# Kernel tuning notes

Hardware: AMD Instinct MI355X
Metric: run time of the kernel (lower is better)

The kernel has to match this reference:

```python
import jax, jax.numpy as jnp
import numpy as np

B, S, N, F, H, E, L = 16, 64, 128, 16, 64, 1024, 2
NEG_SLOPE = 0.2


def _gat_layer(h, src, tgt, Wl, bl, Wr, br, att, bo):
    # h: [B,S,N,H]; src/tgt: [Et] (edges incl. self-loops)
    xl = jnp.einsum('bsnf,hf->bsnh', h, Wl) + bl
    xr = jnp.einsum('bsnf,hf->bsnh', h, Wr) + br
    e = xl[:, :, src] + xr[:, :, tgt]                       # [B,S,Et,H]
    e = jnp.where(e > 0, e, NEG_SLOPE * e)                  # leaky_relu(0.2)
    a = jnp.einsum('bseh,h->bse', e, att)                   # [B,S,Et]
    # segment softmax over target node (stable)
    m = jnp.full(a.shape[:2] + (N,), -jnp.inf, a.dtype).at[:, :, tgt].max(a)
    p = jnp.exp(a - m[:, :, tgt])
    z = jnp.zeros(a.shape[:2] + (N,), a.dtype).at[:, :, tgt].add(p)
    alpha = p / z[:, :, tgt]
    out = jnp.zeros_like(xl).at[:, :, tgt].add(alpha[..., None] * xl[:, :, src])
    return out + bo


def _forward(x, edge_index, in_W, in_b, gat_Wl, gat_bl, gat_Wr, gat_br,
             gat_att, gat_bias, gru_Wih, gru_Whh, gru_bih, gru_bhh,
             oh_W1, oh_b1, oh_W2, oh_b2, dh_W1, dh_b1, dh_W2, dh_b2):
    ar = jnp.arange(N, dtype=edge_index.dtype)
    ei = jnp.concatenate([edge_index, jnp.stack([ar, ar])], axis=1)  # add self-loops
    src, tgt = ei[0], ei[1]
    h = jnp.einsum('bsnf,hf->bsnh', x, in_W) + in_b          # input_proj
    for l in range(L):
        h = jax.nn.relu(_gat_layer(h, src, tgt, gat_Wl[l], gat_bl[l],
                                   gat_Wr[l], gat_br[l], gat_att[l], gat_bias[l]))
    # [B,S,N,H] -> sequences [B*N, S, H]; GRU, keep last state
    seqs = h.transpose(0, 2, 1, 3).reshape(B * N, S, H)

    def step(hprev, xt):
        gi = xt @ gru_Wih.T + gru_bih
        gh = hprev @ gru_Whh.T + gru_bhh
        ir, iz, inn = jnp.split(gi, 3, axis=-1)
        hr, hz, hn = jnp.split(gh, 3, axis=-1)
        r = jax.nn.sigmoid(ir + hr)
        zz = jax.nn.sigmoid(iz + hz)
        n = jnp.tanh(inn + r * hn)
        hnew = (1 - zz) * n + zz * hprev
        return hnew, None

    h0 = jnp.zeros((B * N, H), h.dtype)
    h_last, _ = jax.lax.scan(step, h0, seqs.transpose(1, 0, 2))
    h_last = h_last.reshape(B, N, H)

    def head(hh, W1, b1, W2, b2):
        return jax.nn.relu(hh @ W1.T + b1) @ W2.T + b2

    order = head(h_last, oh_W1, oh_b1, oh_W2, oh_b2)        # [B,N,1]
    demand = head(h_last, dh_W1, dh_b1, dh_W2, dh_b2)       # [B,N,1]
    return order, demand


def setup_inputs() -> dict:
    key = jax.random.key(0)
    ks = jax.random.split(key, 16)
    def g(i, shp, s=0.05):
        return (jax.random.normal(ks[i], shp) * s).astype(jnp.float32)
    x = jax.random.normal(ks[0], (B, S, N, F), dtype=jnp.float32)
    src = jax.random.randint(ks[1], (E,), 0, N)
    off = jax.random.randint(ks[2], (E,), 1, N)
    edge_index = jnp.stack([src, (src + off) % N]).astype(jnp.int32)  # no self-loops
    zf = lambda shp: jnp.zeros(shp, jnp.float32)
    return dict(
        x=x, edge_index=edge_index,
        in_W=g(3, (H, F)), in_b=zf((H,)),
        gat_Wl=g(4, (L, H, H)), gat_bl=zf((L, H)),
        gat_Wr=g(5, (L, H, H)), gat_br=zf((L, H)),
        gat_att=g(6, (L, H), 0.1), gat_bias=zf((L, H)),
        gru_Wih=g(7, (3 * H, H)), gru_Whh=g(8, (3 * H, H)),
        gru_bih=zf((3 * H,)), gru_bhh=zf((3 * H,)),
        oh_W1=g(9, (H // 2, H)), oh_b1=zf((H // 2,)),
        oh_W2=g(10, (1, H // 2)), oh_b2=zf((1,)),
        dh_W1=g(11, (H // 2, H)), dh_b1=zf((H // 2,)),
        dh_W2=g(12, (1, H // 2)), dh_b2=zf((1,)),
    )


def reference(x, edge_index, in_W, in_b, gat_Wl, gat_bl, gat_Wr, gat_br,
              gat_att, gat_bias, gru_Wih, gru_Whh, gru_bih, gru_bhh,
              oh_W1, oh_b1, oh_W2, oh_b2, dh_W1, dh_b1, dh_W2, dh_b2):
    return _forward(x, edge_index, in_W, in_b, gat_Wl, gat_bl, gat_Wr, gat_br,
                    gat_att, gat_bias, gru_Wih, gru_Whh, gru_bih, gru_bhh,
                    oh_W1, oh_b1, oh_W2, oh_b2, dh_W1, dh_b1, dh_W2, dh_b2)
```

## Files before the change

kernel.cpp:

```cpp
#include <hip/hip_runtime.h>
#include <math.h>

#define BB 16
#define SS 64
#define NN 128
#define FF 16
#define HH 64
#define EE 1024
#define ET 1152
#define LLAYERS 2
#define XPAD 65
#define RT (BB * SS * NN)

__device__ __forceinline__ float readlane_f(float v, int k) {
  return __int_as_float(__builtin_amdgcn_readlane(__float_as_int(v), k));
}
__device__ __forceinline__ unsigned flipf(float f) {
  unsigned u = __float_as_uint(f);
  unsigned mask = (u & 0x80000000u) ? 0xFFFFFFFFu : 0x80000000u;
  return u ^ mask;
}
__device__ __forceinline__ float unflipf(unsigned u) {
  unsigned b = (u & 0x80000000u) ? (u ^ 0x80000000u) : ~u;
  return __uint_as_float(b);
}
__device__ __forceinline__ float sigmoidf_(float x) { return 1.f / (1.f + expf(-x)); }

__global__ void setup_csr_kernel(const int* __restrict__ ei,
                                 int* __restrict__ off,
                                 int* __restrict__ csrc,
                                 int* __restrict__ ctgt) {
  __shared__ int deg[NN], cur[NN], offs[NN + 1];
  int tid = threadIdx.x;
  if (tid < NN) deg[tid] = 0;
  __syncthreads();
  for (int e = tid; e < ET; e += 256) {
    int tg = (e < EE) ? ei[EE + e] : (e - EE);
    atomicAdd(&deg[tg], 1);
  }
  __syncthreads();
  if (tid == 0) {
    int s = 0;
    for (int i = 0; i < NN; ++i) { offs[i] = s; s += deg[i]; }
    offs[NN] = s;
  }
  __syncthreads();
  if (tid < NN) cur[tid] = offs[tid];
  if (tid <= NN) off[tid] = offs[tid];
  __syncthreads();
  for (int e = tid; e < ET; e += 256) {
    int sv, tg;
    if (e < EE) { sv = ei[e]; tg = ei[EE + e]; }
    else        { sv = e - EE; tg = e - EE; }
    int pos = atomicAdd(&cur[tg], 1);
    csrc[pos] = sv;
    ctgt[pos] = tg;
  }
}

__global__ __launch_bounds__(256) void input_proj_kernel(
    const float* __restrict__ x, const float* __restrict__ W,
    const float* __restrict__ bvec, float* __restrict__ h) {
  int lane = threadIdx.x & 63;
  int wid = threadIdx.x >> 6;
  float wreg[FF];
#pragma unroll
  for (int i = 0; i < FF / 4; ++i)
    *(float4*)&wreg[4 * i] = ((const float4*)(W + lane * FF))[i];
  float bias = bvec[lane];
  int row0 = __builtin_amdgcn_readfirstlane((blockIdx.x * 4 + wid) * 32);
#pragma unroll 2
  for (int r = 0; r < 32; ++r) {
    int row = row0 + r;
    const float* xr = x + row * FF;
    float acc = bias;
#pragma unroll
    for (int f = 0; f < FF; ++f) acc += xr[f] * wreg[f];
    h[row * HH + lane] = acc;
  }
}

__global__ __launch_bounds__(256) void xlxr_kernel(
    const float* __restrict__ hin,
    const float* __restrict__ Wl, const float* __restrict__ bl,
    const float* __restrict__ Wr, const float* __restrict__ br,
    float* __restrict__ xl, float* __restrict__ xr) {
  int lane = threadIdx.x & 63;
  int wid = (int)threadIdx.x >> 6;
  const float* W  = (wid & 1) ? Wr : Wl;
  const float* bv = (wid & 1) ? br : bl;
  float* outp     = (wid & 1) ? xr : xl;
  float w[HH];
#pragma unroll
  for (int i = 0; i < HH / 4; ++i)
    *(float4*)&w[4 * i] = ((const float4*)(W + lane * HH))[i];
  float bias = bv[lane];
  int row0 = __builtin_amdgcn_readfirstlane(blockIdx.x * 64 + (wid >> 1) * 32);
#pragma unroll 2
  for (int r = 0; r < 32; ++r) {
    const float* hrow = hin + (size_t)(row0 + r) * HH;
    float a0 = bias, a1 = 0.f, a2 = 0.f, a3 = 0.f;
#pragma unroll
    for (int f = 0; f < HH; f += 4) {
      a0 += hrow[f + 0] * w[f + 0];
      a1 += hrow[f + 1] * w[f + 1];
      a2 += hrow[f + 2] * w[f + 2];
      a3 += hrow[f + 3] * w[f + 3];
    }
    outp[(size_t)(row0 + r) * HH + lane] = (a0 + a1) + (a2 + a3);
  }
}

__global__ __launch_bounds__(256) void gat_edge_kernel(
    const float* __restrict__ xl_g, const float* __restrict__ xr_g,
    float* __restrict__ hout,
    const int* __restrict__ csr_off, const int* __restrict__ csr_src,
    const int* __restrict__ csr_tgt,
    const float* __restrict__ att, const float* __restrict__ bo) {
  __shared__ float xl_sh[NN * XPAD];
  __shared__ float xr_sh[NN * XPAD];
  __shared__ float p_sh[ET];
  __shared__ int st_sh[ET];
  __shared__ unsigned m_sh[NN];
  int tid = threadIdx.x, lane = tid & 63, wid = tid >> 6;
  int base = blockIdx.x * (NN * HH);

#pragma unroll 1
  for (int i = tid * 4; i < NN * HH; i += 256 * 4) {
    int row = i >> 6, h = i & 63;
    float4 vl = *(const float4*)(xl_g + base + i);
    float4 vr = *(const float4*)(xr_g + base + i);
    float* dl = xl_sh + row * XPAD + h;
    float* dr = xr_sh + row * XPAD + h;
    dl[0] = vl.x; dl[1] = vl.y; dl[2] = vl.z; dl[3] = vl.w;
    dr[0] = vr.x; dr[1] = vr.y; dr[2] = vr.z; dr[3] = vr.w;
  }
  for (int i = tid; i < ET; i += 256)
    st_sh[i] = csr_src[i] | (csr_tgt[i] << 16);
  if (tid < NN) m_sh[tid] = 0u;
  __syncthreads();

#pragma unroll 1
  for (int e = tid; e < ET; e += 256) {
    int st = st_sh[e];
    int s = st & 0xffff, tg = st >> 16;
    const float* xlr = xl_sh + s * XPAD;
    const float* xrr = xr_sh + tg * XPAD;
    float a0 = 0.f, a1 = 0.f, a2 = 0.f, a3 = 0.f;
#pragma unroll
    for (int h = 0; h < HH; h += 4) {
      float v0 = xlr[h + 0] + xrr[h + 0]; v0 = (v0 > 0.f) ? v0 : 0.2f * v0;
      float v1 = xlr[h + 1] + xrr[h + 1]; v1 = (v1 > 0.f) ? v1 : 0.2f * v1;
      float v2 = xlr[h + 2] + xrr[h + 2]; v2 = (v2 > 0.f) ? v2 : 0.2f * v2;
      float v3 = xlr[h + 3] + xrr[h + 3]; v3 = (v3 > 0.f) ? v3 : 0.2f * v3;
      a0 += v0 * att[h + 0];
      a1 += v1 * att[h + 1];
      a2 += v2 * att[h + 2];
      a3 += v3 * att[h + 3];
    }
    float a = (a0 + a1) + (a2 + a3);
    p_sh[e] = a;
    atomicMax(&m_sh[tg], flipf(a));
  }
  __syncthreads();

  for (int e = tid; e < ET; e += 256) {
    int tg = st_sh[e] >> 16;
    p_sh[e] = expf(p_sh[e] - unflipf(m_sh[tg]));
  }
  __syncthreads();

  float bo_l = bo[lane];
#pragma unroll 1
  for (int n = wid; n < NN; n += 4) {
    int o0 = __builtin_amdgcn_readfirstlane(csr_off[n]);
    int o1 = __builtin_amdgcn_readfirstlane(csr_off[n + 1]);
    float acc = 0.f, z = 0.f;
    for (int i = o0; i < o1; ++i) {
      float p = p_sh[i];
      int s = st_sh[i] & 0xffff;
      acc += p * xl_sh[s * XPAD + lane];
      z += p;
    }
    float o = acc / z + bo_l;
    hout[base + n * HH + lane] = fmaxf(o, 0.f);
  }
}

__device__ __forceinline__ void gemm_half(
    const float* __restrict__ hin, int base,
    const float* __restrict__ W, const float* __restrict__ bvec,
    float* __restrict__ out_sh, int half, int lane) {
  float wreg[HH];
#pragma unroll
  for (int i = 0; i < HH / 4; ++i)
    *(float4*)&wreg[4 * i] = ((const float4*)(W + lane * HH))[i];
  float bias = bvec[lane];
  int n0 = __builtin_amdgcn_readfirstlane(half * 64);
#pragma unroll 1
  for (int nd = 0; nd < 64; ++nd) {
    int node = n0 + nd;
    const float* hrow = hin + base + node * HH;
    float a0 = bias, a1 = 0.f, a2 = 0.f, a3 = 0.f;
#pragma unroll
    for (int f = 0; f < HH; f += 4) {
      a0 += hrow[f + 0] * wreg[f + 0];
      a1 += hrow[f + 1] * wreg[f + 1];
      a2 += hrow[f + 2] * wreg[f + 2];
      a3 += hrow[f + 3] * wreg[f + 3];
    }
    out_sh[node * HH + lane] = (a0 + a1) + (a2 + a3);
  }
}

__global__ __launch_bounds__(256) void gat_fused_kernel(
    const float* __restrict__ hin, float* __restrict__ hout,
    const int* __restrict__ csr_off, const int* __restrict__ csr_src,
    const int* __restrict__ csr_tgt,
    const float* __restrict__ Wl, const float* __restrict__ bl,
    const float* __restrict__ Wr, const float* __restrict__ br,
    const float* __restrict__ att, const float* __restrict__ bo) {
  __shared__ float xl_sh[NN * HH];
  __shared__ float xr_sh[NN * HH];
  __shared__ float p_sh[ET];
  __shared__ int st_sh[ET];
  __shared__ unsigned m_sh[NN];
  int tid = threadIdx.x, lane = tid & 63, wid = tid >> 6;
  int base = blockIdx.x * (NN * HH);

  for (int i = tid; i < ET; i += 256)
    st_sh[i] = csr_src[i] | (csr_tgt[i] << 16);
  if (tid < NN) m_sh[tid] = 0u;

  if (wid < 2) gemm_half(hin, base, Wl, bl, xl_sh, wid & 1, lane);
  else         gemm_half(hin, base, Wr, br, xr_sh, wid & 1, lane);

  float att_l = att[lane];
  float bo_l = bo[lane];
  __syncthreads();

#pragma unroll 1
  for (int e = wid; e < ET; e += 4) {
    int st = st_sh[e];
    int s = st & 0xffff, tg = st >> 16;
    float v = xl_sh[s * HH + lane] + xr_sh[tg * HH + lane];
    v = (v > 0.f) ? v : 0.2f * v;
    float prod = v * att_l;
#pragma unroll
    for (int mm = 32; mm; mm >>= 1) prod += __shfl_xor(prod, mm);
    if (lane == 0) {
      p_sh[e] = prod;
      atomicMax(&m_sh[tg], flipf(prod));
    }
  }
  __syncthreads();

  for (int e = tid; e < ET; e += 256) {
    int tg = st_sh[e] >> 16;
    p_sh[e] = expf(p_sh[e] - unflipf(m_sh[tg]));
  }
  __syncthreads();

#pragma unroll 1
  for (int n = wid; n < NN; n += 4) {
    int o0 = csr_off[n], o1 = csr_off[n + 1];
    float acc = 0.f, z = 0.f;
    for (int i = o0; i < o1; ++i) {
      float p = p_sh[i];
      int s = st_sh[i] & 0xffff;
      acc += p * xl_sh[s * HH + lane];
      z += p;
    }
    float o = acc / z + bo_l;
    hout[base + n * HH + lane] = fmaxf(o, 0.f);
  }
}

__global__ __launch_bounds__(192) void gi_proj_kernel(
    const float* __restrict__ hin, const float* __restrict__ Wih,
    const float* __restrict__ bih, float* __restrict__ gi) {
  int lane = threadIdx.x & 63;
  int w = (int)threadIdx.x >> 6;
  float wreg[HH];
  const float4* wsrc = (const float4*)(Wih + (size_t)(w * 64 + lane) * HH);
#pragma unroll
  for (int i = 0; i < HH / 4; ++i) *(float4*)&wreg[4 * i] = wsrc[i];
  float bias = bih[w * 64 + lane];
  int row0 = __builtin_amdgcn_readfirstlane(blockIdx.x * 64);
#pragma unroll 2
  for (int r = 0; r < 64; ++r) {
    int row = row0 + r;
    const float* hrow = hin + (size_t)row * HH;
    float a0 = bias, a1 = 0.f, a2 = 0.f, a3 = 0.f;
#pragma unroll
    for (int f = 0; f < HH; f += 4) {
      a0 += hrow[f + 0] * wreg[f + 0];
      a1 += hrow[f + 1] * wreg[f + 1];
      a2 += hrow[f + 2] * wreg[f + 2];
      a3 += hrow[f + 3] * wreg[f + 3];
    }
    gi[(size_t)row * 192 + w * 64 + lane] = (a0 + a1) + (a2 + a3);
  }
}

__global__ __launch_bounds__(64, 2) void gru_rec_kernel(
    const float* __restrict__ gi,
    const float* __restrict__ Whh, const float* __restrict__ bhh,
    const float* __restrict__ oW1, const float* __restrict__ ob1,
    const float* __restrict__ oW2, const float* __restrict__ ob2,
    const float* __restrict__ dW1, const float* __restrict__ db1,
    const float* __restrict__ dW2, const float* __restrict__ db2,
    float* __restrict__ out) {
  int lane = threadIdx.x;
  int seq = blockIdx.x;
  int b = seq >> 7, n = seq & (NN - 1);

  float wr[HH], wz[HH], wn[HH];
  {
    const float4* s0 = (const float4*)(Whh + (size_t)(0 * 64 + lane) * HH);
    const float4* s1 = (const float4*)(Whh + (size_t)(1 * 64 + lane) * HH);
    const float4* s2 = (const float4*)(Whh + (size_t)(2 * 64 + lane) * HH);
#pragma unroll
    for (int i = 0; i < HH / 4; ++i) {
      *(float4*)&wr[4 * i] = s0[i];
      *(float4*)&wz[4 * i] = s1[i];
      *(float4*)&wn[4 * i] = s2[i];
    }
  }
  float br_ = bhh[lane], bz_ = bhh[64 + lane], bn_ = bhh[128 + lane];

  const float* gbase = gi + ((size_t)b * SS * NN + (size_t)n) * 192;
  float gir = gbase[lane], giz = gbase[64 + lane], gin = gbase[128 + lane];
  const float* g1 = gbase + (size_t)NN * 192;
  float pir = g1[lane], piz = g1[64 + lane], pin = g1[128 + lane];
  float hj = 0.f;

#pragma unroll 1
  for (int t = 0; t < SS; ++t) {
    float qir = 0.f, qiz = 0.f, qin = 0.f;
    if (t + 2 < SS) {
      const float* g2 = gbase + (size_t)(t + 2) * NN * 192;
      qir = g2[lane]; qiz = g2[64 + lane]; qin = g2[128 + lane];
    }
    float ar0 = br_, ar1 = 0.f, az0 = bz_, az1 = 0.f, an0 = bn_, an1 = 0.f;
#pragma unroll
    for (int k = 0; k < HH; k += 2) {
      float h0 = readlane_f(hj, k), h1 = readlane_f(hj, k + 1);
      ar0 += h0 * wr[k];     az0 += h0 * wz[k];     an0 += h0 * wn[k];
      ar1 += h1 * wr[k + 1]; az1 += h1 * wz[k + 1]; an1 += h1 * wn[k + 1];
    }
    float r  = sigmoidf_(gir + ar0 + ar1);
    float z  = sigmoidf_(giz + az0 + az1);
    float nn_ = tanhf(gin + r * (an0 + an1));
    hj = (1.f - z) * nn_ + z * hj;
    gir = pir; giz = piz; gin = pin;
    pir = qir; piz = qiz; pin = qin;
  }

  int half = lane >> 5, jp = lane & 31;
  const float* W1 = half ? dW1 : oW1;
  const float* b1 = half ? db1 : ob1;
  const float* W2 = half ? dW2 : oW2;
  const float* b2 = half ? db2 : ob2;
  float wv[HH];
#pragma unroll
  for (int i = 0; i < HH / 4; ++i)
    *(float4*)&wv[4 * i] = ((const float4*)(W1 + jp * HH))[i];
  float acc = b1[jp];
#pragma unroll
  for (int k = 0; k < HH; ++k)
    acc += readlane_f(hj, k) * wv[k];
  float val = fmaxf(acc, 0.f) * W2[jp];
  val += __shfl_down(val, 16, 32);
  val += __shfl_down(val, 8, 32);
  val += __shfl_down(val, 4, 32);
  val += __shfl_down(val, 2, 32);
  val += __shfl_down(val, 1, 32);
  if (jp == 0) out[half * (BB * NN) + seq] = val + b2[0];
}

__global__ __launch_bounds__(192, 3) void gru_fused_kernel(
    const float* __restrict__ hbuf,
    const float* __restrict__ Wih, const float* __restrict__ Whh,
    const float* __restrict__ bih, const float* __restrict__ bhh,
    const float* __restrict__ oW1, const float* __restrict__ ob1,
    const float* __restrict__ oW2, const float* __restrict__ ob2,
    const float* __restrict__ dW1, const float* __restrict__ db1,
    const float* __restrict__ dW2, const float* __restrict__ db2,
    float* __restrict__ out) {
  __shared__ float gi_sh[SS * 3 * HH];
  __shared__ float exch[2][3][HH];

  int lane = threadIdx.x & 63;
  int g = (int)threadIdx.x >> 6;
  int seq = blockIdx.x;
  int b = seq >> 7, n = seq & (NN - 1);
  const float* xbase = hbuf + ((size_t)b * SS * NN + (size_t)n) * HH;

  {
    float w[HH];
    const float4* wsrc = (const float4*)(Wih + (size_t)(g * 64 + lane) * HH);
#pragma unroll
    for (int i = 0; i < HH / 4; ++i) *(float4*)&w[4 * i] = wsrc[i];
    float bias = bih[g * 64 + lane];
#pragma unroll 2
    for (int t = 0; t < SS; ++t) {
      const float* xr = xbase + (size_t)t * NN * HH;
      float a0 = bias, a1 = 0.f, a2 = 0.f, a3 = 0.f;
#pragma unroll
      for (int k = 0; k < HH; k += 4) {
        float4 xb = *(const float4*)(xr + k);
        a0 += xb.x * w[k + 0];
        a1 += xb.y * w[k + 1];
        a2 += xb.z * w[k + 2];
        a3 += xb.w * w[k + 3];
      }
      gi_sh[(t * 3 + g) * HH + lane] = (a0 + a1) + (a2 + a3);
    }
  }

  float whh[HH];
  {
    const float4* wsrc = (const float4*)(Whh + (size_t)(g * 64 + lane) * HH);
#pragma unroll
    for (int i = 0; i < HH / 4; ++i) *(float4*)&whh[4 * i] = wsrc[i];
  }
  float bhg = bhh[g * 64 + lane];
  float hj = 0.f;
  __syncthreads();

#pragma unroll 1
  for (int t = 0; t < SS; ++t) {
    float a0 = bhg, a1 = 0.f, a2 = 0.f, a3 = 0.f;
#pragma unroll
    for (int k = 0; k < HH; k += 4) {
      a0 += readlane_f(hj, k + 0) * whh[k + 0];
      a1 += readlane_f(hj, k + 1) * whh[k + 1];
      a2 += readlane_f(hj, k + 2) * whh[k + 2];
      a3 += readlane_f(hj, k + 3) * whh[k + 3];
    }
    float gh = (a0 + a1) + (a2 + a3);
    int slot = t & 1;
    exch[slot][g][lane] = gh;
    __syncthreads();
    float ghr = exch[slot][0][lane];
    float ghz = exch[slot][1][lane];
    float ghn = exch[slot][2][lane];
    float gir = gi_sh[(t * 3 + 0) * HH + lane];
    float giz = gi_sh[(t * 3 + 1) * HH + lane];
    float gin = gi_sh[(t * 3 + 2) * HH + lane];
    float r  = sigmoidf_(gir + ghr);
    float z  = sigmoidf_(giz + ghz);
    float nn_ = tanhf(gin + r * ghn);
    hj = (1.f - z) * nn_ + z * hj;
  }

  if (g == 0) {
    int half = lane >> 5, jp = lane & 31;
    const float* W1 = half ? dW1 : oW1;
    const float* b1 = half ? db1 : ob1;
    const float* W2 = half ? dW2 : oW2;
    const float* b2 = half ? db2 : ob2;
    float wv[HH];
#pragma unroll
    for (int i = 0; i < HH / 4; ++i)
      *(float4*)&wv[4 * i] = ((const float4*)(W1 + jp * HH))[i];
    float acc = b1[jp];
#pragma unroll
    for (int k = 0; k < HH; ++k)
      acc += readlane_f(hj, k) * wv[k];
    float val = fmaxf(acc, 0.f) * W2[jp];
    val += __shfl_down(val, 16, 32);
    val += __shfl_down(val, 8, 32);
    val += __shfl_down(val, 4, 32);
    val += __shfl_down(val, 2, 32);
    val += __shfl_down(val, 1, 32);
    if (jp == 0) out[half * (BB * NN) + seq] = val + b2[0];
  }
}

extern "C" void kernel_launch(void* const* d_in, const int* in_sizes, int n_in,
                              void* d_out, int out_size, void* d_ws, size_t ws_size,
                              hipStream_t stream) {
  const float* x       = (const float*)d_in[0];
  const int*   ei      = (const int*)d_in[1];
  const float* in_W    = (const float*)d_in[2];
  const float* in_b    = (const float*)d_in[3];
  const float* gat_Wl  = (const float*)d_in[4];
  const float* gat_bl  = (const float*)d_in[5];
  const float* gat_Wr  = (const float*)d_in[6];
  const float* gat_br  = (const float*)d_in[7];
  const float* gat_att = (const float*)d_in[8];
  const float* gat_bias= (const float*)d_in[9];
  const float* gru_Wih = (const float*)d_in[10];
  const float* gru_Whh = (const float*)d_in[11];
  const float* gru_bih = (const float*)d_in[12];
  const float* gru_bhh = (const float*)d_in[13];
  const float* oh_W1   = (const float*)d_in[14];
  const float* oh_b1   = (const float*)d_in[15];
  const float* oh_W2   = (const float*)d_in[16];
  const float* oh_b2   = (const float*)d_in[17];
  const float* dh_W1   = (const float*)d_in[18];
  const float* dh_b1   = (const float*)d_in[19];
  const float* dh_W2   = (const float*)d_in[20];
  const float* dh_b2   = (const float*)d_in[21];
  float* out = (float*)d_out;

  char* ws = (char*)d_ws;
  size_t hfloats = (size_t)BB * SS * NN * HH;
  float* hbuf = (float*)ws;
  size_t off_csr = hfloats * sizeof(float);
  size_t off_buf = off_csr + (160 + 2 * ET) * sizeof(int);
  off_buf = (off_buf + 255) & ~(size_t)255;
  int* csr_off = (int*)(ws + off_csr);
  int* csr_src = csr_off + 160;
  int* csr_tgt = csr_src + ET;
  float* xlbuf = (float*)(ws + off_buf);
  float* xrbuf = xlbuf + hfloats;
  size_t need_gat = off_buf + 2 * hfloats * sizeof(float);
  bool big_gat = (ws_size >= need_gat);
  float* gibuf = (float*)(ws + off_buf);
  size_t need_gru = off_buf + (size_t)RT * 192 * sizeof(float);
  bool big_gru = (ws_size >= need_gru);

  setup_csr_kernel<<<1, 256, 0, stream>>>(ei, csr_off, csr_src, csr_tgt);
  input_proj_kernel<<<(BB * SS * NN) / (4 * 32), 256, 0, stream>>>(x, in_W, in_b, hbuf);
  for (int l = 0; l < LLAYERS; ++l) {
    if (big_gat) {
      xlxr_kernel<<<(BB * SS * NN) / 64, 256, 0, stream>>>(
          hbuf, gat_Wl + l * HH * HH, gat_bl + l * HH,
          gat_Wr + l * HH * HH, gat_br + l * HH, xlbuf, xrbuf);
      gat_edge_kernel<<<BB * SS, 256, 0, stream>>>(
          xlbuf, xrbuf, hbuf, csr_off, csr_src, csr_tgt,
          gat_att + l * HH, gat_bias + l * HH);
    } else {
      gat_fused_kernel<<<BB * SS, 256, 0, stream>>>(
          hbuf, hbuf, csr_off, csr_src, csr_tgt,
          gat_Wl + l * HH * HH, gat_bl + l * HH,
          gat_Wr + l * HH * HH, gat_br + l * HH,
          gat_att + l * HH, gat_bias + l * HH);
    }
  }
  if (big_gru) {
    gi_proj_kernel<<<RT / 64, 192, 0, stream>>>(hbuf, gru_Wih, gru_bih, gibuf);
    gru_rec_kernel<<<BB * NN, 64, 0, stream>>>(
        gibuf, gru_Whh, gru_bhh,
        oh_W1, oh_b1, oh_W2, oh_b2, dh_W1, dh_b1, dh_W2, dh_b2, out);
  } else {
    gru_fused_kernel<<<BB * NN, 192, 0, stream>>>(
        hbuf, gru_Wih, gru_Whh, gru_bih, gru_bhh,
        oh_W1, oh_b1, oh_W2, oh_b2, dh_W1, dh_b1, dh_W2, dh_b2, out);
  }
}
```

Before: 750.3 us.

## Stage hidden rows in LDS and compute multiple projections per thread

xlxr and gi_proj kernels now use single-wavefront blocks. Each block stages a 64-row tile of h into shared memory, and each thread holds all weight rows for its output column (both Wl/Wr, or all three GRU gates), so each h element read is reused across several outputs with float4 LDS loads. The GRU recurrence replaces 64 readlane broadcasts per step with a shared-memory h vector plus a barrier per step. The change raises register pressure (up to 192 weight floats per thread) and lowers threads per block, which risks occupancy and spilling.

```diff
diff --git a/kernel.cpp b/kernel.cpp
--- a/kernel.cpp
+++ b/kernel.cpp
@@ -80,34 +80,47 @@
   }
 }
 
-__global__ __launch_bounds__(256) void xlxr_kernel(
+__global__ __launch_bounds__(64, 2) void xlxr_kernel(
     const float* __restrict__ hin,
     const float* __restrict__ Wl, const float* __restrict__ bl,
     const float* __restrict__ Wr, const float* __restrict__ br,
     float* __restrict__ xl, float* __restrict__ xr) {
-  int lane = threadIdx.x & 63;
-  int wid = (int)threadIdx.x >> 6;
-  const float* W  = (wid & 1) ? Wr : Wl;
-  const float* bv = (wid & 1) ? br : bl;
-  float* outp     = (wid & 1) ? xr : xl;
-  float w[HH];
-#pragma unroll
-  for (int i = 0; i < HH / 4; ++i)
-    *(float4*)&w[4 * i] = ((const float4*)(W + lane * HH))[i];
-  float bias = bv[lane];
-  int row0 = __builtin_amdgcn_readfirstlane(blockIdx.x * 64 + (wid >> 1) * 32);
+  __shared__ float hsh[64][HH];
+  int j = threadIdx.x;
+  float wl_[HH], wr_[HH];
+  {
+    const float4* sl = (const float4*)(Wl + (size_t)j * HH);
+    const float4* sr = (const float4*)(Wr + (size_t)j * HH);
+#pragma unroll
+    for (int i = 0; i < HH / 4; ++i) {
+      *(float4*)&wl_[4 * i] = sl[i];
+      *(float4*)&wr_[4 * i] = sr[i];
+    }
+  }
+  float blj = bl[j], brj = br[j];
+  int row0 = blockIdx.x * 64;
+  {
+    const float4* src = (const float4*)(hin + (size_t)row0 * HH);
+    float4* dst = (float4*)hsh;
+#pragma unroll
+    for (int i = 0; i < 16; ++i)
+      dst[i * 64 + j] = src[i * 64 + j];
+  }
+  __syncthreads();
 #pragma unroll 2
-  for (int r = 0; r < 32; ++r) {
-    const float* hrow = hin + (size_t)(row0 + r) * HH;
-    float a0 = bias, a1 = 0.f, a2 = 0.f, a3 = 0.f;
-#pragma unroll
-    for (int f = 0; f < HH; f += 4) {
-      a0 += hrow[f + 0] * w[f + 0];
-      a1 += hrow[f + 1] * w[f + 1];
-      a2 += hrow[f + 2] * w[f + 2];
-      a3 += hrow[f + 3] * w[f + 3];
-    }
-    outp[(size_t)(row0 + r) * HH + lane] = (a0 + a1) + (a2 + a3);
+  for (int r = 0; r < 64; ++r) {
+    float al0 = blj, al1 = 0.f, ar0 = brj, ar1 = 0.f;
+#pragma unroll
+    for (int k = 0; k < HH; k += 4) {
+      float4 hb = *(const float4*)&hsh[r][k];
+      al0 += hb.x * wl_[k + 0]; ar0 += hb.x * wr_[k + 0];
+      al1 += hb.y * wl_[k + 1]; ar1 += hb.y * wr_[k + 1];
+      al0 += hb.z * wl_[k + 2]; ar0 += hb.z * wr_[k + 2];
+      al1 += hb.w * wl_[k + 3]; ar1 += hb.w * wr_[k + 3];
+    }
+    size_t o = (size_t)(row0 + r) * HH + j;
+    xl[o] = al0 + al1;
+    xr[o] = ar0 + ar1;
   }
 }
 
@@ -276,30 +289,48 @@
   }
 }
 
-__global__ __launch_bounds__(192) void gi_proj_kernel(
+__global__ __launch_bounds__(64, 2) void gi_proj_kernel(
     const float* __restrict__ hin, const float* __restrict__ Wih,
     const float* __restrict__ bih, float* __restrict__ gi) {
-  int lane = threadIdx.x & 63;
-  int w = (int)threadIdx.x >> 6;
-  float wreg[HH];
-  const float4* wsrc = (const float4*)(Wih + (size_t)(w * 64 + lane) * HH);
-#pragma unroll
-  for (int i = 0; i < HH / 4; ++i) *(float4*)&wreg[4 * i] = wsrc[i];
-  float bias = bih[w * 64 + lane];
-  int row0 = __builtin_amdgcn_readfirstlane(blockIdx.x * 64);
+  __shared__ float hsh[64][HH];
+  int j = threadIdx.x;
+  float wr[HH], wz[HH], wn[HH];
+  {
+    const float4* s0 = (const float4*)(Wih + (size_t)(0 * 64 + j) * HH);
+    const float4* s1 = (const float4*)(Wih + (size_t)(1 * 64 + j) * HH);
+    const float4* s2 = (const float4*)(Wih + (size_t)(2 * 64 + j) * HH);
+#pragma unroll
+    for (int i = 0; i < HH / 4; ++i) {
+      *(float4*)&wr[4 * i] = s0[i];
+      *(float4*)&wz[4 * i] = s1[i];
+      *(float4*)&wn[4 * i] = s2[i];
+    }
+  }
+  float br_ = bih[j], bz_ = bih[64 + j], bn_ = bih[128 + j];
+  int row0 = blockIdx.x * 64;
+  {
+    const float4* src = (const float4*)(hin + (size_t)row0 * HH);
+    float4* dst = (float4*)hsh;
+#pragma unroll
+    for (int i = 0; i < 16; ++i)
+      dst[i * 64 + j] = src[i * 64 + j];
+  }
+  __syncthreads();
 #pragma unroll 2
   for (int r = 0; r < 64; ++r) {
-    int row = row0 + r;
-    const float* hrow = hin + (size_t)row * HH;
-    float a0 = bias, a1 = 0.f, a2 = 0.f, a3 = 0.f;
-#pragma unroll
-    for (int f = 0; f < HH; f += 4) {
-      a0 += hrow[f + 0] * wreg[f + 0];
-      a1 += hrow[f + 1] * wreg[f + 1];
-      a2 += hrow[f + 2] * wreg[f + 2];
-      a3 += hrow[f + 3] * wreg[f + 3];
-    }
-    gi[(size_t)row * 192 + w * 64 + lane] = (a0 + a1) + (a2 + a3);
+    float ar0 = br_, ar1 = 0.f, az0 = bz_, az1 = 0.f, an0 = bn_, an1 = 0.f;
+#pragma unroll
+    for (int k = 0; k < HH; k += 4) {
+      float4 hb = *(const float4*)&hsh[r][k];
+      ar0 += hb.x * wr[k + 0]; az0 += hb.x * wz[k + 0]; an0 += hb.x * wn[k + 0];
+      ar1 += hb.y * wr[k + 1]; az1 += hb.y * wz[k + 1]; an1 += hb.y * wn[k + 1];
+      ar0 += hb.z * wr[k + 2]; az0 += hb.z * wz[k + 2]; an0 += hb.z * wn[k + 2];
+      ar1 += hb.w * wr[k + 3]; az1 += hb.w * wz[k + 3]; an1 += hb.w * wn[k + 3];
+    }
+    size_t o = (size_t)(row0 + r) * 192;
+    gi[o + j]       = ar0 + ar1;
+    gi[o + 64 + j]  = az0 + az1;
+    gi[o + 128 + j] = an0 + an1;
   }
 }
 
@@ -311,6 +342,7 @@
     const float* __restrict__ dW1, const float* __restrict__ db1,
     const float* __restrict__ dW2, const float* __restrict__ db2,
     float* __restrict__ out) {
+  __shared__ float hsh[HH];
   int lane = threadIdx.x;
   int seq = blockIdx.x;
   int b = seq >> 7, n = seq & (NN - 1);
@@ -334,6 +366,8 @@
   const float* g1 = gbase + (size_t)NN * 192;
   float pir = g1[lane], piz = g1[64 + lane], pin = g1[128 + lane];
   float hj = 0.f;
+  hsh[lane] = 0.f;
+  __syncthreads();
 
 #pragma unroll 1
   for (int t = 0; t < SS; ++t) {
@@ -344,15 +378,19 @@
     }
     float ar0 = br_, ar1 = 0.f, az0 = bz_, az1 = 0.f, an0 = bn_, an1 = 0.f;
 #pragma unroll
-    for (int k = 0; k < HH; k += 2) {
-      float h0 = readlane_f(hj, k), h1 = readlane_f(hj, k + 1);
-      ar0 += h0 * wr[k];     az0 += h0 * wz[k];     an0 += h0 * wn[k];
-      ar1 += h1 * wr[k + 1]; az1 += h1 * wz[k + 1]; an1 += h1 * wn[k + 1];
+    for (int k = 0; k < HH; k += 4) {
+      float4 hb = *(const float4*)(hsh + k);
+      ar0 += hb.x * wr[k + 0]; az0 += hb.x * wz[k + 0]; an0 += hb.x * wn[k + 0];
+      ar1 += hb.y * wr[k + 1]; az1 += hb.y * wz[k + 1]; an1 += hb.y * wn[k + 1];
+      ar0 += hb.z * wr[k + 2]; az0 += hb.z * wz[k + 2]; an0 += hb.z * wn[k + 2];
+      ar1 += hb.w * wr[k + 3]; az1 += hb.w * wz[k + 3]; an1 += hb.w * wn[k + 3];
     }
     float r  = sigmoidf_(gir + ar0 + ar1);
     float z  = sigmoidf_(giz + az0 + az1);
     float nn_ = tanhf(gin + r * (an0 + an1));
     hj = (1.f - z) * nn_ + z * hj;
+    hsh[lane] = hj;
+    __syncthreads();
     gir = pir; giz = piz; gin = pin;
     pir = qir; piz = qiz; pin = qin;
   }
@@ -368,8 +406,13 @@
     *(float4*)&wv[4 * i] = ((const float4*)(W1 + jp * HH))[i];
   float acc = b1[jp];
 #pragma unroll
-  for (int k = 0; k < HH; ++k)
-    acc += readlane_f(hj, k) * wv[k];
+  for (int k = 0; k < HH; k += 4) {
+    float4 hb = *(const float4*)(hsh + k);
+    acc += hb.x * wv[k + 0];
+    acc += hb.y * wv[k + 1];
+    acc += hb.z * wv[k + 2];
+    acc += hb.w * wv[k + 3];
+  }
   float val = fmaxf(acc, 0.f) * W2[jp];
   val += __shfl_down(val, 16, 32);
   val += __shfl_down(val, 8, 32);
@@ -527,7 +570,7 @@
   input_proj_kernel<<<(BB * SS * NN) / (4 * 32), 256, 0, stream>>>(x, in_W, in_b, hbuf);
   for (int l = 0; l < LLAYERS; ++l) {
     if (big_gat) {
-      xlxr_kernel<<<(BB * SS * NN) / 64, 256, 0, stream>>>(
+      xlxr_kernel<<<RT / 64, 64, 0, stream>>>(
           hbuf, gat_Wl + l * HH * HH, gat_bl + l * HH,
           gat_Wr + l * HH * HH, gat_br + l * HH, xlbuf, xrbuf);
       gat_edge_kernel<<<BB * SS, 256, 0, stream>>>(
@@ -542,7 +585,7 @@
     }
   }
   if (big_gru) {
-    gi_proj_kernel<<<RT / 64, 192, 0, stream>>>(hbuf, gru_Wih, gru_bih, gibuf);
+    gi_proj_kernel<<<RT / 64, 64, 0, stream>>>(hbuf, gru_Wih, gru_bih, gibuf);
     gru_rec_kernel<<<BB * NN, 64, 0, stream>>>(
         gibuf, gru_Whh, gru_bhh,
         oh_W1, oh_b1, oh_W2, oh_b2, dh_W1, dh_b1, dh_W2, dh_b2, out);
```

Result: slower. 1.773 ms (+136.4%).
